# Kernel tuning notes

Hardware: AMD Instinct MI355X
Metric: run time of the kernel (lower is better)

Reference implementation:

```python
import jax, jax.numpy as jnp
import numpy as np

VOCAB = 50257
D_EMB = 128
HIDDEN = 256
N_CLS = 2
B, T = 256, 2048


def setup_inputs() -> dict:
    key = jax.random.key(0)
    ks = jax.random.split(key, 8)
    batch = jax.random.randint(ks[0], (B, T), 0, VOCAB, dtype=jnp.int64) if jax.config.jax_enable_x64 else jax.random.randint(ks[0], (B, T), 0, VOCAB, dtype=jnp.int32)
    emb_table = jax.random.normal(ks[1], (VOCAB, D_EMB), dtype=jnp.float32) * 0.02
    emb_table = emb_table.at[0].set(0.0)  # padding_idx=0
    sx = 1.0 / np.sqrt(D_EMB)
    sh = 1.0 / np.sqrt(HIDDEN)
    wx_w = jax.random.uniform(ks[2], (D_EMB, HIDDEN), jnp.float32, -sx, sx)
    wx_b = jax.random.uniform(ks[3], (HIDDEN,), jnp.float32, -sx, sx)
    wh_w = jax.random.uniform(ks[4], (HIDDEN, HIDDEN), jnp.float32, -sh, sh)
    wh_b = jax.random.uniform(ks[5], (HIDDEN,), jnp.float32, -sh, sh)
    clf_w = jax.random.uniform(ks[6], (HIDDEN, N_CLS), jnp.float32, -sh, sh)
    clf_b = jax.random.uniform(ks[7], (N_CLS,), jnp.float32, -sh, sh)
    return {"batch": batch, "emb_table": emb_table, "wx_w": wx_w, "wx_b": wx_b,
            "wh_w": wh_w, "wh_b": wh_b, "clf_w": clf_w, "clf_b": clf_b}


def reference(batch, emb_table, wx_w, wx_b, wh_w, wh_b, clf_w, clf_b):
    # emb: [B, T, D_EMB]
    emb = emb_table[batch]
    b, t, d = emb.shape
    h0 = jnp.zeros((b, wh_w.shape[0]), dtype=emb.dtype)
    # Precompute wx(x) for all timesteps in one big GEMM (same math,
    # hoists the time-invariant contraction out of the sequential loop).
    ax = jnp.einsum('btd,dh->bth', emb, wx_w) + wx_b  # [B, T, H]

    def step(h, a_t):
        h_new = jnp.tanh(a_t + h @ wh_w + wh_b)
        return h_new, None

    h_final, _ = jax.lax.scan(step, h0, jnp.swapaxes(ax, 0, 1))  # scan over T
    return h_final @ clf_w + clf_b  # [B, 2]
```

## Files before the change

### kernel.cpp

```cpp
#include <hip/hip_runtime.h>
#include <hip/hip_bf16.h>

#define VOCAB  50257
#define D_EMB  128
#define HID    256
#define N_CLS  2
#define BSZ    256
#define T_LEN  2048

typedef float f16v __attribute__((ext_vector_type(16)));

__global__ __launch_bounds__(256)
void tabax_kernel(const float* __restrict__ emb,
                  const float* __restrict__ wxw,
                  const float* __restrict__ wxb,
                  const float* __restrict__ whb,
                  float* __restrict__ tab)
{
    const int j  = threadIdx.x;
    const int v0 = blockIdx.x * 32;
    const int rows = min(32, VOCAB - v0);

    __shared__ float ebuf[32 * D_EMB];
    for (int i = j; i < rows * D_EMB; i += 256)
        ebuf[i] = emb[(size_t)v0 * D_EMB + i];
    __syncthreads();

    float acc[32];
#pragma unroll
    for (int r = 0; r < 32; ++r) acc[r] = 0.f;

#pragma unroll 8
    for (int d = 0; d < D_EMB; ++d) {
        float wxv = wxw[d * HID + j];
#pragma unroll
        for (int r = 0; r < 32; ++r)
            acc[r] = fmaf(ebuf[r * D_EMB + d], wxv, acc[r]);
    }

    const float bb = wxb[j] + whb[j];
    for (int r = 0; r < rows; ++r)
        tab[(size_t)(v0 + r) * HID + j] = acc[r] + bb;
}

__device__ __forceinline__ float fast_tanh(float x) {
    float e2 = __expf(2.f * x);
    float r  = __builtin_amdgcn_rcpf(e2 + 1.f);
    return fmaf(-2.f, r, 1.f);
}

#define DPP_ADD_ROR8(DST, SEND, KEEP)                                       \
    asm("v_add_f32 %0, %1, %2 row_ror:8 row_mask:0xf bank_mask:0xf"         \
        : "=v"(DST) : "v"(SEND), "v"(KEEP))
#define DPP_ADD_HMIR(DST, SEND, KEEP)                                       \
    asm("v_add_f32 %0, %1, %2 row_half_mirror row_mask:0xf bank_mask:0xf"   \
        : "=v"(DST) : "v"(SEND), "v"(KEEP))
#define DPP_QADD1(ACC)                                                      \
    asm("v_add_f32 %0, %0, %0 quad_perm:[1,0,3,2] row_mask:0xf "            \
        "bank_mask:0xf" : "+v"(ACC))
#define DPP_QADD2(ACC)                                                      \
    asm("v_add_f32 %0, %0, %0 quad_perm:[2,3,0,1] row_mask:0xf "            \
        "bank_mask:0xf" : "+v"(ACC))

__global__ __launch_bounds__(1024, 1)
void rnn_main_kernel(const int*   __restrict__ batch,
                     const float* __restrict__ whw,
                     const float* __restrict__ clfw,
                     const float* __restrict__ clfb,
                     const float* __restrict__ ax_tab,
                     float*       __restrict__ out)
{
    const int b   = blockIdx.x;
    const int tid = threadIdx.x;
    const int kg  = tid & 15;
    const int cg  = tid >> 4;
    const int c0  = cg * 4;
    const int kb  = kg * 16;
    const int rot = (kg >> 2) & 3;

    __shared__ float hbuf[2][HID];
    __shared__ float sbuf[2][HID];

    f16v Wt[4];
#pragma unroll
    for (int e = 0; e < 4; ++e) {
        const int swz = (e + rot) & 3;
#pragma unroll
        for (int m = 0; m < 4; ++m) {
            const int k = kb + swz * 4 + m;
            const float4 w4 = *(const float4*)&whw[(size_t)k * HID + c0];
            Wt[e][m * 4 + 0] = w4.x;
            Wt[e][m * 4 + 1] = w4.y;
            Wt[e][m * 4 + 2] = w4.z;
            Wt[e][m * 4 + 3] = w4.w;
        }
    }
    asm volatile("" : "+v"(Wt[0]));
    asm volatile("" : "+v"(Wt[1]));
    asm volatile("" : "+v"(Wt[2]));
    asm volatile("" : "+v"(Wt[3]));

    int lds_off[4];
#pragma unroll
    for (int e = 0; e < 4; ++e) lds_off[e] = kg * 64 + ((e + rot) & 3) * 16;

    const int  mycol = c0 + (kg >> 2);
    const bool wr    = (kg & 3) == 0;

    if (tid < HID) hbuf[0][tid] = 0.f;

    const int* brow = batch + (size_t)b * T_LEN;
    const float* axp = ax_tab + mycol;
    int tok_n = brow[0];
    float axv = axp[(unsigned)tok_n * 256u];
    tok_n = brow[1];
    __syncthreads();

#define RNN_STEP(CUR, NXT, TT)                                              \
    {                                                                       \
        const int tok_nn = ((TT) + 2 < T_LEN) ? brow[(TT) + 2] : 0;         \
        const float ax_n = axp[(unsigned)tok_n * 256u];                     \
        float acc[4];                                                       \
        const char* hb = (const char*)&hbuf[CUR][0];                        \
        {                                        \
            const float4 h4 = *(const float4*)(hb + lds_off[0]);            \
            const float hm[4] = {h4.x, h4.y, h4.z, h4.w};                   \
            _Pragma("unroll")                                               \
            for (int i = 0; i < 4; ++i) acc[i] = hm[0] * Wt[0][i];          \
            _Pragma("unroll")                                               \
            for (int m = 1; m < 4; ++m)                                     \
                _Pragma("unroll")                                           \
                for (int i = 0; i < 4; ++i)                                 \
                    acc[i] = fmaf(hm[m], Wt[0][m * 4 + i], acc[i]);         \
        }                                                                   \
        _Pragma("unroll")                                                   \
        for (int e = 1; e < 4; ++e) {                                       \
            const float4 h4 = *(const float4*)(hb + lds_off[e]);            \
            const float hm[4] = {h4.x, h4.y, h4.z, h4.w};                   \
            _Pragma("unroll")                                               \
            for (int m = 0; m < 4; ++m)                                     \
                _Pragma("unroll")                                           \
                for (int i = 0; i < 4; ++i)                                 \
                    acc[i] = fmaf(hm[m], Wt[e][m * 4 + i], acc[i]);         \
        }                                                                   \
                                \
        const bool hi8 = (kg & 8) != 0;                                     \
        const float sA = hi8 ? acc[0] : acc[2];                             \
        const float kA = hi8 ? acc[2] : acc[0];                             \
        const float sB = hi8 ? acc[1] : acc[3];                             \
        const float kB = hi8 ? acc[3] : acc[1];                             \
        float accA, accB;                                                   \
        DPP_ADD_ROR8(accA, sA, kA);                                         \
        DPP_ADD_ROR8(accB, sB, kB);                                         \
                \
        const bool hi4 = (kg & 4) != 0;                                     \
        const float sC = hi4 ? accA : accB;                                 \
        const float kC = hi4 ? accB : accA;                                 \
        float accQ;                                                         \
        DPP_ADD_HMIR(accQ, sC, kC);                                         \
           \
        DPP_QADD1(accQ);                                                    \
        DPP_QADD2(accQ);                                                    \
        const float hnew = fast_tanh(accQ + axv);                           \
        if (wr) hbuf[NXT][mycol] = hnew;                                    \
        __syncthreads();                                                    \
        axv   = ax_n;                                                       \
        tok_n = tok_nn;                                                     \
    }

    for (int t = 0; t < T_LEN; t += 2) {
        RNN_STEP(0, 1, t)
        RNN_STEP(1, 0, t + 1)
    }
#undef RNN_STEP

    if (tid < HID) {
        const float h = hbuf[0][tid];
        sbuf[0][tid] = h * clfw[tid * N_CLS + 0];
        sbuf[1][tid] = h * clfw[tid * N_CLS + 1];
    }
    __syncthreads();
    if (tid < 64) {
        float v = sbuf[0][tid] + sbuf[0][tid + 64] +
                  sbuf[0][tid + 128] + sbuf[0][tid + 192];
#pragma unroll
        for (int off = 32; off > 0; off >>= 1) v += __shfl_xor(v, off);
        if (tid == 0) out[b * N_CLS + 0] = v + clfb[0];
    } else if (tid < 128) {
        const int l = tid - 64;
        float v = sbuf[1][l] + sbuf[1][l + 64] +
                  sbuf[1][l + 128] + sbuf[1][l + 192];
#pragma unroll
        for (int off = 32; off > 0; off >>= 1) v += __shfl_xor(v, off);
        if (l == 0) out[b * N_CLS + 1] = v + clfb[1];
    }
}

__global__ __launch_bounds__(512, 2)
void rnn_fallback_kernel(const int*   __restrict__ batch,
                         const float* __restrict__ emb,
                         const float* __restrict__ wxw,
                         const float* __restrict__ wxb,
                         const float* __restrict__ whw,
                         const float* __restrict__ whb,
                         const float* __restrict__ clfw,
                         const float* __restrict__ clfb,
                         float*       __restrict__ out)
{
    const int b    = blockIdx.x;
    const int tid  = threadIdx.x;
    const int j    = tid >> 1;
    const int half = tid & 1;
    const int k0   = half * 128;

    __shared__ float hbuf[2][HID];
    __shared__ float ebuf[2][D_EMB];

    float w[128];
#pragma unroll
    for (int k = 0; k < 128; ++k)
        w[k] = whw[(size_t)(k0 + k) * HID + j];

    float wx[64];
#pragma unroll
    for (int d = 0; d < 64; ++d)
        wx[d] = wxw[(size_t)(half * 64 + d) * HID + j];

    const float bj  = whb[j];
    const float axb = wxb[j];

    if (tid < HID) hbuf[0][tid] = 0.f;

    const int* brow = batch + (size_t)b * T_LEN;

    int tok_n = brow[0];
    if (tid < D_EMB) ebuf[0][tid] = emb[(size_t)tok_n * D_EMB + tid];
    tok_n = brow[1];
    __syncthreads();

    float h_j = 0.f;
    int cur = 0;
    for (int t = 0; t < T_LEN; ++t) {
        const int nxt = cur ^ 1;
        const int tok_nn = (t + 2 < T_LEN) ? brow[t + 2] : 0;
        float ev = 0.f;
        if (t + 1 < T_LEN && tid < D_EMB)
            ev = emb[(size_t)tok_n * D_EMB + tid];

        float a0 = 0.f, a1 = 0.f, a2 = 0.f, a3 = 0.f;
        const float4* hv = (const float4*)&hbuf[cur][k0];
#pragma unroll
        for (int i = 0; i < 32; ++i) {
            float4 h4 = hv[i];
            a0 = fmaf(h4.x, w[4 * i + 0], a0);
            a1 = fmaf(h4.y, w[4 * i + 1], a1);
            a2 = fmaf(h4.z, w[4 * i + 2], a2);
            a3 = fmaf(h4.w, w[4 * i + 3], a3);
        }
        const float4* evv = (const float4*)&ebuf[cur][half * 64];
#pragma unroll
        for (int i = 0; i < 16; ++i) {
            float4 e4 = evv[i];
            a0 = fmaf(e4.x, wx[4 * i + 0], a0);
            a1 = fmaf(e4.y, wx[4 * i + 1], a1);
            a2 = fmaf(e4.z, wx[4 * i + 2], a2);
            a3 = fmaf(e4.w, wx[4 * i + 3], a3);
        }
        float s = (a0 + a1) + (a2 + a3);
        s += __shfl_xor(s, 1);

        h_j = fast_tanh(s + bj + axb);

        if (half == 0) hbuf[nxt][j] = h_j;
        if (t + 1 < T_LEN && tid < D_EMB) ebuf[nxt][tid] = ev;
        __syncthreads();

        tok_n = tok_nn;
        cur   = nxt;
    }

    if (half == 0) {
        hbuf[0][j] = h_j * clfw[j * N_CLS + 0];
        hbuf[1][j] = h_j * clfw[j * N_CLS + 1];
    }
    __syncthreads();
    if (tid < 64) {
        float v = hbuf[0][tid] + hbuf[0][tid + 64] +
                  hbuf[0][tid + 128] + hbuf[0][tid + 192];
#pragma unroll
        for (int off = 32; off > 0; off >>= 1) v += __shfl_xor(v, off);
        if (tid == 0) out[b * N_CLS + 0] = v + clfb[0];
    } else if (tid < 128) {
        const int l = tid - 64;
        float v = hbuf[1][l] + hbuf[1][l + 64] +
                  hbuf[1][l + 128] + hbuf[1][l + 192];
#pragma unroll
        for (int off = 32; off > 0; off >>= 1) v += __shfl_xor(v, off);
        if (l == 0) out[b * N_CLS + 1] = v + clfb[1];
    }
}

extern "C" void kernel_launch(void* const* d_in, const int* in_sizes, int n_in,
                              void* d_out, int out_size, void* d_ws, size_t ws_size,
                              hipStream_t stream)
{
    const int*   batch = (const int*)  d_in[0];
    const float* emb   = (const float*)d_in[1];
    const float* wxw   = (const float*)d_in[2];
    const float* wxb   = (const float*)d_in[3];
    const float* whw   = (const float*)d_in[4];
    const float* whb   = (const float*)d_in[5];
    const float* clfw  = (const float*)d_in[6];
    const float* clfb  = (const float*)d_in[7];
    float* out = (float*)d_out;

    const size_t tab_bytes = (size_t)VOCAB * HID * sizeof(float);
    if (ws_size >= tab_bytes) {
        float* tab = (float*)d_ws;
        tabax_kernel<<<(VOCAB + 31) / 32, 256, 0, stream>>>(emb, wxw, wxb, whb, tab);
        rnn_main_kernel<<<BSZ, 1024, 0, stream>>>(batch, whw, clfw, clfb, tab, out);
    } else {
        rnn_fallback_kernel<<<BSZ, 512, 0, stream>>>(batch, emb, wxw, wxb, whw, whb,
                                                     clfw, clfb, out);
    }
}
```

Before: 1.181 ms.

## Halve RNN block size so each thread computes eight hidden columns

The recurrent kernel now launches 512 threads per batch row instead of 1024. Each thread keeps an 8-column slice of the recurrent weight matrix in registers, split into two register arrays. The cross-lane DPP reduction is rebuilt to reduce eight partial sums across 16 lanes, so that two lanes end up owning each output column. The aim is a cheaper per-step barrier with fewer waves and more independent FMAs per thread. In exchange, register pressure roughly doubles and fewer waves are available to hide latency on each SIMD.

```diff
diff --git a/kernel.cpp b/kernel.cpp
--- a/kernel.cpp
+++ b/kernel.cpp
@@ -55,14 +55,14 @@
 #define DPP_ADD_HMIR(DST, SEND, KEEP)                                       \
     asm("v_add_f32 %0, %1, %2 row_half_mirror row_mask:0xf bank_mask:0xf"   \
         : "=v"(DST) : "v"(SEND), "v"(KEEP))
+#define DPP_ADD_X2(DST, SEND, KEEP)                                         \
+    asm("v_add_f32 %0, %1, %2 quad_perm:[2,3,0,1] row_mask:0xf "            \
+        "bank_mask:0xf" : "=v"(DST) : "v"(SEND), "v"(KEEP))
 #define DPP_QADD1(ACC)                                                      \
     asm("v_add_f32 %0, %0, %0 quad_perm:[1,0,3,2] row_mask:0xf "            \
         "bank_mask:0xf" : "+v"(ACC))
-#define DPP_QADD2(ACC)                                                      \
-    asm("v_add_f32 %0, %0, %0 quad_perm:[2,3,0,1] row_mask:0xf "            \
-        "bank_mask:0xf" : "+v"(ACC))
-
-__global__ __launch_bounds__(1024, 1)
+
+__global__ __launch_bounds__(512, 1)
 void rnn_main_kernel(const int*   __restrict__ batch,
                      const float* __restrict__ whw,
                      const float* __restrict__ clfw,
@@ -74,38 +74,43 @@
     const int tid = threadIdx.x;
     const int kg  = tid & 15;
     const int cg  = tid >> 4;
-    const int c0  = cg * 4;
+    const int c0  = cg * 8;
     const int kb  = kg * 16;
     const int rot = (kg >> 2) & 3;
 
     __shared__ float hbuf[2][HID];
     __shared__ float sbuf[2][HID];
 
-    f16v Wt[4];
+    f16v WtA[4], WtB[4];
 #pragma unroll
     for (int e = 0; e < 4; ++e) {
         const int swz = (e + rot) & 3;
 #pragma unroll
         for (int m = 0; m < 4; ++m) {
             const int k = kb + swz * 4 + m;
-            const float4 w4 = *(const float4*)&whw[(size_t)k * HID + c0];
-            Wt[e][m * 4 + 0] = w4.x;
-            Wt[e][m * 4 + 1] = w4.y;
-            Wt[e][m * 4 + 2] = w4.z;
-            Wt[e][m * 4 + 3] = w4.w;
+            const float4 wlo = *(const float4*)&whw[(size_t)k * HID + c0];
+            const float4 whi = *(const float4*)&whw[(size_t)k * HID + c0 + 4];
+            WtA[e][m * 4 + 0] = wlo.x; WtA[e][m * 4 + 1] = wlo.y;
+            WtA[e][m * 4 + 2] = wlo.z; WtA[e][m * 4 + 3] = wlo.w;
+            WtB[e][m * 4 + 0] = whi.x; WtB[e][m * 4 + 1] = whi.y;
+            WtB[e][m * 4 + 2] = whi.z; WtB[e][m * 4 + 3] = whi.w;
         }
     }
-    asm volatile("" : "+v"(Wt[0]));
-    asm volatile("" : "+v"(Wt[1]));
-    asm volatile("" : "+v"(Wt[2]));
-    asm volatile("" : "+v"(Wt[3]));
+    asm volatile("" : "+v"(WtA[0]));
+    asm volatile("" : "+v"(WtA[1]));
+    asm volatile("" : "+v"(WtA[2]));
+    asm volatile("" : "+v"(WtA[3]));
+    asm volatile("" : "+v"(WtB[0]));
+    asm volatile("" : "+v"(WtB[1]));
+    asm volatile("" : "+v"(WtB[2]));
+    asm volatile("" : "+v"(WtB[3]));
 
     int lds_off[4];
 #pragma unroll
     for (int e = 0; e < 4; ++e) lds_off[e] = kg * 64 + ((e + rot) & 3) * 16;
 
-    const int  mycol = c0 + (kg >> 2);
-    const bool wr    = (kg & 3) == 0;
+    const int  mycol = c0 + ((kg >> 3) << 2) + ((kg >> 2) & 1) + (kg & 2);
+    const bool wr    = (kg & 1) == 0;
 
     if (tid < HID) hbuf[0][tid] = 0.f;
 
@@ -120,18 +125,23 @@
     {                                                                       \
         const int tok_nn = ((TT) + 2 < T_LEN) ? brow[(TT) + 2] : 0;         \
         const float ax_n = axp[(unsigned)tok_n * 256u];                     \
-        float acc[4];                                                       \
+        float accA[4], accB[4];                                             \
         const char* hb = (const char*)&hbuf[CUR][0];                        \
-        {                                        \
+        {                                \
             const float4 h4 = *(const float4*)(hb + lds_off[0]);            \
             const float hm[4] = {h4.x, h4.y, h4.z, h4.w};                   \
             _Pragma("unroll")                                               \
-            for (int i = 0; i < 4; ++i) acc[i] = hm[0] * Wt[0][i];          \
+            for (int i = 0; i < 4; ++i) {                                   \
+                accA[i] = hm[0] * WtA[0][i];                                \
+                accB[i] = hm[0] * WtB[0][i];                                \
+            }                                                               \
             _Pragma("unroll")                                               \
             for (int m = 1; m < 4; ++m)                                     \
                 _Pragma("unroll")                                           \
-                for (int i = 0; i < 4; ++i)                                 \
-                    acc[i] = fmaf(hm[m], Wt[0][m * 4 + i], acc[i]);         \
+                for (int i = 0; i < 4; ++i) {                               \
+                    accA[i] = fmaf(hm[m], WtA[0][m * 4 + i], accA[i]);      \
+                    accB[i] = fmaf(hm[m], WtB[0][m * 4 + i], accB[i]);      \
+                }                                                           \
         }                                                                   \
         _Pragma("unroll")                                                   \
         for (int e = 1; e < 4; ++e) {                                       \
@@ -140,28 +150,50 @@
             _Pragma("unroll")                                               \
             for (int m = 0; m < 4; ++m)                                     \
                 _Pragma("unroll")                                           \
-                for (int i = 0; i < 4; ++i)                                 \
-                    acc[i] = fmaf(hm[m], Wt[e][m * 4 + i], acc[i]);         \
-        }                                                                   \
-                                \
+                for (int i = 0; i < 4; ++i) {                               \
+                    accA[i] = fmaf(hm[m], WtA[e][m * 4 + i], accA[i]);      \
+                    accB[i] = fmaf(hm[m], WtB[e][m * 4 + i], accB[i]);      \
+                }                                                           \
+        }                                                                   \
+            \
         const bool hi8 = (kg & 8) != 0;                                     \
-        const float sA = hi8 ? acc[0] : acc[2];                             \
-        const float kA = hi8 ? acc[2] : acc[0];                             \
-        const float sB = hi8 ? acc[1] : acc[3];                             \
-        const float kB = hi8 ? acc[3] : acc[1];                             \
-        float accA, accB;                                                   \
-        DPP_ADD_ROR8(accA, sA, kA);                                         \
-        DPP_ADD_ROR8(accB, sB, kB);                                         \
-                \
+        float P0, P1, P2, P3;                                               \
+        {                                                                   \
+            const float s0 = hi8 ? accA[0] : accB[0];                       \
+            const float k0 = hi8 ? accB[0] : accA[0];                       \
+            DPP_ADD_ROR8(P0, s0, k0);                                       \
+            const float s1 = hi8 ? accA[1] : accB[1];                       \
+            const float k1 = hi8 ? accB[1] : accA[1];                       \
+            DPP_ADD_ROR8(P1, s1, k1);                                       \
+            const float s2 = hi8 ? accA[2] : accB[2];                       \
+            const float k2 = hi8 ? accB[2] : accA[2];                       \
+            DPP_ADD_ROR8(P2, s2, k2);                                       \
+            const float s3 = hi8 ? accA[3] : accB[3];                       \
+            const float k3 = hi8 ? accB[3] : accA[3];                       \
+            DPP_ADD_ROR8(P3, s3, k3);                                       \
+        }                                                                   \
+                                              \
         const bool hi4 = (kg & 4) != 0;                                     \
-        const float sC = hi4 ? accA : accB;                                 \
-        const float kC = hi4 ? accB : accA;                                 \
-        float accQ;                                                         \
-        DPP_ADD_HMIR(accQ, sC, kC);                                         \
-           \
-        DPP_QADD1(accQ);                                                    \
-        DPP_QADD2(accQ);                                                    \
-        const float hnew = fast_tanh(accQ + axv);                           \
+        float Q1, Q2;                                                       \
+        {                                                                   \
+            const float s1 = hi4 ? P0 : P1;                                 \
+            const float k1 = hi4 ? P1 : P0;                                 \
+            DPP_ADD_HMIR(Q1, s1, k1);                                       \
+            const float s2 = hi4 ? P2 : P3;                                 \
+            const float k2 = hi4 ? P3 : P2;                                 \
+            DPP_ADD_HMIR(Q2, s2, k2);                                       \
+        }                                                                   \
+                                                \
+        const bool hi2 = (kg & 2) != 0;                                     \
+        float R;                                                            \
+        {                                                                   \
+            const float s = hi2 ? Q1 : Q2;                                  \
+            const float k = hi2 ? Q2 : Q1;                                  \
+            DPP_ADD_X2(R, s, k);                                            \
+        }                                                                   \
+                               \
+        DPP_QADD1(R);                                                       \
+        const float hnew = fast_tanh(R + axv);                              \
         if (wr) hbuf[NXT][mycol] = hnew;                                    \
         __syncthreads();                                                    \
         axv   = ax_n;                                                       \
@@ -318,7 +350,7 @@
     if (ws_size >= tab_bytes) {
         float* tab = (float*)d_ws;
         tabax_kernel<<<(VOCAB + 31) / 32, 256, 0, stream>>>(emb, wxw, wxb, whb, tab);
-        rnn_main_kernel<<<BSZ, 1024, 0, stream>>>(batch, whw, clfw, clfb, tab, out);
+        rnn_main_kernel<<<BSZ, 512, 0, stream>>>(batch, whw, clfw, clfb, tab, out);
     } else {
         rnn_fallback_kernel<<<BSZ, 512, 0, stream>>>(batch, emb, wxw, wxb, whw, whb,
                                                      clfw, clfb, out);
```

Measured after the change: 1.178 ms. No clear change (-0.2%).
